# Kernel optimization log

Hardware: AMD Instinct MI355X
Metric: run time of the kernel (lower is better)

The kernel has to match this reference:

```python
import jax, jax.numpy as jnp
import numpy as np

NUM_HEADS = 16
ROPE_BASE = 10000.0

def rotate_half(x):
    h = x.shape[-1] // 2
    return jnp.concatenate([-x[..., h:], x[..., :h]], axis=-1)

def rope_cos_sin(seq_len, head_dim, dtype):
    inv_freq = 1.0 / (ROPE_BASE ** (jnp.arange(0, head_dim, 2, dtype=jnp.float32) / head_dim))
    t = jnp.arange(seq_len, dtype=jnp.float32)
    freqs = jnp.outer(t, inv_freq)              # [N, hd/2]
    emb = jnp.concatenate([freqs, freqs], -1)   # [N, hd]
    return jnp.cos(emb).astype(dtype), jnp.sin(emb).astype(dtype)

def setup_inputs() -> dict:
    key = jax.random.key(0)
    ks = jax.random.split(key, 5)
    B, N, D = 2, 2048, 1024
    s = 1.0 / np.sqrt(D)
    return {
        "x": jax.random.normal(ks[0], (B, N, D), jnp.float32),
        "attention_mask": jnp.ones((B, N), jnp.int32),
        "Wq": jax.random.normal(ks[1], (D, D), jnp.float32) * s,
        "Wk": jax.random.normal(ks[2], (D, D), jnp.float32) * s,
        "Wv": jax.random.normal(ks[3], (D, D), jnp.float32) * s,
        "Wo": jax.random.normal(ks[4], (D, D), jnp.float32) * s,
    }

def reference(x, attention_mask, Wq, Wk, Wv, Wo):
    B, N, D = x.shape
    H = NUM_HEADS
    hd = D // H
    scale = hd ** -0.5
    # projections (nn.Linear: x @ W.T), split heads -> [B, H, N, hd]
    q = jnp.einsum('bnd,ed->bne', x, Wq).reshape(B, N, H, hd).transpose(0, 2, 1, 3)
    k = jnp.einsum('bnd,ed->bne', x, Wk).reshape(B, N, H, hd).transpose(0, 2, 1, 3)
    v = jnp.einsum('bnd,ed->bne', x, Wv).reshape(B, N, H, hd).transpose(0, 2, 1, 3)
    cos, sin = rope_cos_sin(N, hd, x.dtype)     # [N, hd]
    cos = cos[None, None]; sin = sin[None, None]
    q = q * cos + rotate_half(q) * sin
    k = k * cos + rotate_half(k) * sin
    attn = jnp.einsum('bhqd,bhkd->bhqk', q, k) * scale
    mask = attention_mask.astype(bool)[:, None, None, :]        # [B,1,1,N]
    attn = jnp.where(mask, attn, -jnp.inf)
    all_masked = (attention_mask.sum(-1) == 0)[:, None, None, None]
    attn = jnp.where(all_masked, 0.0, attn)
    attn = jax.nn.softmax(attn, axis=-1)
    out = jnp.einsum('bhqk,bhkd->bhqd', attn, v)
    out = out.transpose(0, 2, 1, 3).reshape(B, N, D)
    return jnp.einsum('bnd,ed->bne', out, Wo)
```

## Files before the change

### kernel.cpp

```cpp
#include <hip/hip_runtime.h>
#include <math.h>

#define BATCH 2
#define SEQ   2048
#define DM    1024
#define NH    16
#define HD    64
#define MTOT  (BATCH*SEQ)

typedef short v8s __attribute__((ext_vector_type(8)));
typedef short v4s __attribute__((ext_vector_type(4)));
typedef float v4f __attribute__((ext_vector_type(4)));

#define MFMA16(a, b, c) __builtin_amdgcn_mfma_f32_16x16x32_bf16((a), (b), (c), 0, 0, 0)

__device__ __forceinline__ short f2b(float f) {
    union { float f; unsigned u; } v; v.f = f;
    return (short)((v.u + 0x8000u) >> 16);
}

__device__ __forceinline__ void rope_cs(int n, float f_rev, float* c, float* s) {
    float rev = (float)n * f_rev;
    float t = rev - floorf(rev);
    float ang = t * 6.283185307179586f;
    *c = __cosf(ang);
    *s = __sinf(ang);
}

#define L2_1E4_D32 0.4152410118609203f
#define INV2PI     0.15915494309189535f

__global__ __launch_bounds__(256) void cvt_all_kernel(
    const float* __restrict__ x,  const float* __restrict__ wq,
    const float* __restrict__ wk, const float* __restrict__ wv,
    const float* __restrict__ wo, short* __restrict__ dst)
{
    int i = blockIdx.x * 256 + threadIdx.x;
    const float* src; int off;
    if (i < (1 << 19)) { src = x; off = i; }
    else {
        int j = i - (1 << 19);
        int wsel = j >> 17;
        off = j & ((1 << 17) - 1);
        src = (wsel == 0) ? wq : (wsel == 1) ? wk : (wsel == 2) ? wv : wo;
    }
    const float4* s4 = (const float4*)src;
    float4 a = s4[2 * off], b = s4[2 * off + 1];
    v8s p;
    p[0] = f2b(a.x); p[1] = f2b(a.y); p[2] = f2b(a.z); p[3] = f2b(a.w);
    p[4] = f2b(b.x); p[5] = f2b(b.y); p[6] = f2b(b.z); p[7] = f2b(b.w);
    *(v8s*)&dst[8 * i] = p;
}

__global__ __launch_bounds__(256, 2) void kv_rope_mfma(
    const short* __restrict__ xb, const short* __restrict__ Wkb,
    const short* __restrict__ Wvb, short* __restrict__ K, short* __restrict__ Vt)
{
    const int zz = blockIdx.z;
    const short* __restrict__ Wb = zz ? Wvb : Wkb;
    const int m0 = blockIdx.x * 128, e00 = blockIdx.y * 128;
    const int tid = threadIdx.x;
    const int w = tid >> 6, lane = tid & 63, lq = lane >> 4, lr = lane & 15;
    const int wm = w >> 1, wn = w & 1;

    __shared__ union {
        struct { short As[128][32]; short Bs[128][32]; } p1;
        short Css[128][136];
    } u;

    v4f acc[4][4];
    #pragma unroll
    for (int i = 0; i < 4; ++i)
        for (int j = 0; j < 4; ++j)
            for (int r = 0; r < 4; ++r) acc[i][j][r] = 0.f;

    const int arow = tid >> 1, aseg = (tid & 1) * 16;
    for (int k0 = 0; k0 < DM; k0 += 32) {
        v8s a0 = *(const v8s*)&xb[(size_t)(m0 + arow) * DM + k0 + aseg];
        v8s a1 = *(const v8s*)&xb[(size_t)(m0 + arow) * DM + k0 + aseg + 8];
        v8s b0 = *(const v8s*)&Wb[(size_t)(e00 + arow) * DM + k0 + aseg];
        v8s b1 = *(const v8s*)&Wb[(size_t)(e00 + arow) * DM + k0 + aseg + 8];
        __syncthreads();
        *(v8s*)&u.p1.As[arow][aseg] = a0;
        *(v8s*)&u.p1.As[arow][aseg + 8] = a1;
        *(v8s*)&u.p1.Bs[arow][aseg] = b0;
        *(v8s*)&u.p1.Bs[arow][aseg + 8] = b1;
        __syncthreads();
        v8s af[4], bf[4];
        #pragma unroll
        for (int i = 0; i < 4; ++i)
            af[i] = *(const v8s*)&u.p1.As[64 * wm + 16 * i + lr][8 * lq];
        #pragma unroll
        for (int j = 0; j < 4; ++j)
            bf[j] = *(const v8s*)&u.p1.Bs[64 * wn + 16 * j + lr][8 * lq];
        #pragma unroll
        for (int i = 0; i < 4; ++i)
            #pragma unroll
            for (int j = 0; j < 4; ++j)
                acc[i][j] = MFMA16(af[i], bf[j], acc[i][j]);
    }
    __syncthreads();

    const int b = m0 >> 11, n00 = m0 & (SEQ - 1);

    if (zz == 0) {
        float f0 = exp2f(-(float)lr * L2_1E4_D32) * INV2PI;
        float f1 = exp2f(-(float)(16 + lr) * L2_1E4_D32) * INV2PI;
        #pragma unroll
        for (int i = 0; i < 4; ++i) {
            #pragma unroll
            for (int r = 0; r < 4; ++r) {
                int row = 64 * wm + 16 * i + 4 * lq + r;
                int n = n00 + row;
                float c0v, s0v, c1v, s1v;
                rope_cs(n, f0, &c0v, &s0v);
                rope_cs(n, f1, &c1v, &s1v);
                float q0 = acc[i][0][r], q1 = acc[i][1][r];
                float q2 = acc[i][2][r], q3 = acc[i][3][r];
                u.Css[row][64 * wn + lr]      = f2b(q0 * c0v - q2 * s0v);
                u.Css[row][64 * wn + 16 + lr] = f2b(q1 * c1v - q3 * s1v);
                u.Css[row][64 * wn + 32 + lr] = f2b(q2 * c0v + q0 * s0v);
                u.Css[row][64 * wn + 48 + lr] = f2b(q3 * c1v + q1 * s1v);
            }
        }
        __syncthreads();
        int row = tid >> 1, hh = tid & 1;
        int h = (e00 >> 6) + hh;
        int n = n00 + row;
        size_t base = (((size_t)(b * NH + h)) * SEQ + n) * HD;
        #pragma unroll
        for (int p = 0; p < 8; ++p)
            *(v8s*)&K[base + 8 * p] = *(const v8s*)&u.Css[row][64 * hh + 8 * p];
    } else {
        #pragma unroll
        for (int i = 0; i < 4; ++i) {
            #pragma unroll
            for (int j = 0; j < 4; ++j) {
                v4s t;
                #pragma unroll
                for (int r = 0; r < 4; ++r) t[r] = f2b(acc[i][j][r]);
                *(v4s*)&u.Css[64 * wn + 16 * j + lr][64 * wm + 16 * i + 4 * lq] = t;
            }
        }
        __syncthreads();
        int c = tid >> 1, half = (tid & 1) * 64;
        int h = (e00 + c) >> 6, d = (e00 + c) & 63;
        size_t base = (((size_t)(b * NH + h)) * HD + d) * SEQ + n00 + half;
        #pragma unroll
        for (int p = 0; p < 8; ++p)
            *(v8s*)&Vt[base + 8 * p] = *(const v8s*)&u.Css[c][half + 8 * p];
    }
}

__global__ __launch_bounds__(512, 4) void attn_mfma(
    const short* __restrict__ xb, const short* __restrict__ Wqb,
    const short* __restrict__ K, const short* __restrict__ Vt,
    const int* __restrict__ mask, short* __restrict__ O)
{
    const int m0 = blockIdx.x * 128, h = blockIdx.y, e0 = h * 64;
    const int b = m0 >> 11, n0 = m0 & (SEQ - 1), bh = b * NH + h;
    const int tid = threadIdx.x;
    const int w = tid >> 6, lane = tid & 63, lq = lane >> 4, lr = lane & 15;

    __shared__ union {
        struct { short As[128][32]; short Bs[64][32]; } p1;
        struct { short Ks[64][72]; short Vs[64][72]; } p2;
    } u;
    __shared__ short Ps[128][72];
    __shared__ float mbias[64];

    v4f acc[4];
    #pragma unroll
    for (int nt = 0; nt < 4; ++nt)
        for (int r = 0; r < 4; ++r) acc[nt][r] = 0.f;

    const int sr = tid >> 2, sc = (tid & 3) * 8;
    const int br = (tid - 256) >> 2, bc = (tid & 3) * 8;
    for (int k0 = 0; k0 < DM; k0 += 32) {
        v8s a0 = *(const v8s*)&xb[(size_t)(m0 + sr) * DM + k0 + sc];
        v8s bv;
        if (tid >= 256)
            bv = *(const v8s*)&Wqb[(size_t)(e0 + br) * DM + k0 + bc];
        __syncthreads();
        *(v8s*)&u.p1.As[sr][sc] = a0;
        if (tid >= 256)
            *(v8s*)&u.p1.Bs[br][bc] = bv;
        __syncthreads();
        v8s aw = *(const v8s*)&u.p1.As[16 * w + lr][8 * lq];
        #pragma unroll
        for (int nt = 0; nt < 4; ++nt) {
            v8s bb = *(const v8s*)&u.p1.Bs[16 * nt + lr][8 * lq];
            acc[nt] = MFMA16(aw, bb, acc[nt]);
        }
    }

    {
        const float QSCALE = 0.18033688011112042f;
        float f0 = exp2f(-(float)lr * L2_1E4_D32) * INV2PI;
        float f1 = exp2f(-(float)(16 + lr) * L2_1E4_D32) * INV2PI;
        #pragma unroll
        for (int r = 0; r < 4; ++r) {
            int row = 16 * w + 4 * lq + r;
            int n = n0 + row;
            float c0v, s0v, c1v, s1v;
            rope_cs(n, f0, &c0v, &s0v);
            rope_cs(n, f1, &c1v, &s1v);
            float q0 = acc[0][r], q1 = acc[1][r];
            float q2 = acc[2][r], q3 = acc[3][r];
            Ps[row][lr]      = f2b(QSCALE * (q0 * c0v - q2 * s0v));
            Ps[row][16 + lr] = f2b(QSCALE * (q1 * c1v - q3 * s1v));
            Ps[row][32 + lr] = f2b(QSCALE * (q2 * c0v + q0 * s0v));
            Ps[row][48 + lr] = f2b(QSCALE * (q3 * c1v + q1 * s1v));
        }
    }
    v8s aq[2];
    #pragma unroll
    for (int ks = 0; ks < 2; ++ks)
        aq[ks] = *(const v8s*)&Ps[16 * w + lr][32 * ks + 8 * lq];

    float lacc[4] = {0.f, 0.f, 0.f, 0.f};
    v4f o[4];
    #pragma unroll
    for (int nt = 0; nt < 4; ++nt)
        for (int r = 0; r < 4; ++r) o[nt][r] = 0.f;

    const int kr = tid >> 3, kc = (tid & 7) * 8;
    const int pr = 16 * (kr & 3) + (kr >> 2);
    const short* __restrict__ Kb = K + (size_t)bh * SEQ * HD;
    const short* __restrict__ Vb = Vt + (size_t)bh * HD * SEQ;

    v8s k1 = *(const v8s*)&Kb[(size_t)kr * HD + kc];
    v8s v1 = *(const v8s*)&Vb[(size_t)kr * SEQ + kc];
    int mnext = (tid < 64) ? mask[b * SEQ + tid] : 0;

    for (int c0 = 0; c0 < SEQ; c0 += 64) {
        __syncthreads();
        *(v8s*)&u.p2.Ks[pr][kc] = k1;
        *(v8s*)&u.p2.Vs[kr][kc] = v1;
        if (tid < 64) mbias[tid] = mnext ? -24.0f : -1e30f;
        __syncthreads();
        if (c0 + 64 < SEQ) {
            k1 = *(const v8s*)&Kb[(size_t)(c0 + 64 + kr) * HD + kc];
            v1 = *(const v8s*)&Vb[(size_t)kr * SEQ + c0 + 64 + kc];
            if (tid < 64) mnext = mask[b * SEQ + c0 + 64 + tid];
        }

        v8s kf[2][4], vf[2][4];
        #pragma unroll
        for (int ks = 0; ks < 2; ++ks)
            #pragma unroll
            for (int nt = 0; nt < 4; ++nt) {
                kf[ks][nt] = *(const v8s*)&u.p2.Ks[16 * nt + lr][32 * ks + 8 * lq];
                vf[ks][nt] = *(const v8s*)&u.p2.Vs[16 * nt + lr][32 * ks + 8 * lq];
            }
        float bias[4];
        #pragma unroll
        for (int nt = 0; nt < 4; ++nt) bias[nt] = mbias[4 * lr + nt];

        v4f sv[4];
        #pragma unroll
        for (int nt = 0; nt < 4; ++nt)
            for (int r = 0; r < 4; ++r) sv[nt][r] = 0.f;
        #pragma unroll
        for (int ks = 0; ks < 2; ++ks)
            #pragma unroll
            for (int nt = 0; nt < 4; ++nt)
                sv[nt] = MFMA16(aq[ks], kf[ks][nt], sv[nt]);

        #pragma unroll
        for (int r = 0; r < 4; ++r) {
            v4s pk;
            #pragma unroll
            for (int nt = 0; nt < 4; ++nt) {
                float p = exp2f(sv[nt][r] + bias[nt]);
                lacc[r] += p;
                pk[nt] = f2b(p);
            }
            *(v4s*)&Ps[16 * w + 4 * lq + r][4 * lr] = pk;
        }
        #pragma unroll
        for (int ks = 0; ks < 2; ++ks) {
            v8s a = *(const v8s*)&Ps[16 * w + lr][32 * ks + 8 * lq];
            #pragma unroll
            for (int nt = 0; nt < 4; ++nt)
                o[nt] = MFMA16(a, vf[ks][nt], o[nt]);
        }
    }

    #pragma unroll
    for (int r = 0; r < 4; ++r) {
        float l = lacc[r];
        l += __shfl_xor(l, 1);
        l += __shfl_xor(l, 2);
        l += __shfl_xor(l, 4);
        l += __shfl_xor(l, 8);
        float inv = (l > 0.f) ? 1.f / l : 0.f;
        int qrow = 16 * w + 4 * lq + r;
        #pragma unroll
        for (int nt = 0; nt < 4; ++nt)
            O[(size_t)(m0 + qrow) * DM + h * HD + 16 * nt + lr] =
                f2b(o[nt][r] * inv);
    }
}

__global__ __launch_bounds__(256, 2) void oproj_mfma(
    const short* __restrict__ O, const short* __restrict__ Wob,
    float* __restrict__ out)
{
    const int m0 = blockIdx.x * 64, e00 = blockIdx.y * 128;
    const int tid = threadIdx.x;
    const int w = tid >> 6, lane = tid & 63, lq = lane >> 4, lr = lane & 15;

    __shared__ short As[64][32];
    __shared__ short Bs[128][32];

    v4f acc[4][2];
    #pragma unroll
    for (int i = 0; i < 4; ++i)
        for (int j = 0; j < 2; ++j)
            for (int r = 0; r < 4; ++r) acc[i][j][r] = 0.f;

    const int arow = tid >> 2, aseg = (tid & 3) * 8;
    const int brow = tid >> 1, bseg = (tid & 1) * 16;
    for (int k0 = 0; k0 < DM; k0 += 32) {
        v8s a0 = *(const v8s*)&O[(size_t)(m0 + arow) * DM + k0 + aseg];
        v8s b0 = *(const v8s*)&Wob[(size_t)(e00 + brow) * DM + k0 + bseg];
        v8s b1 = *(const v8s*)&Wob[(size_t)(e00 + brow) * DM + k0 + bseg + 8];
        __syncthreads();
        *(v8s*)&As[arow][aseg] = a0;
        *(v8s*)&Bs[brow][bseg] = b0;
        *(v8s*)&Bs[brow][bseg + 8] = b1;
        __syncthreads();
        v8s af[4], bf[2];
        #pragma unroll
        for (int i = 0; i < 4; ++i)
            af[i] = *(const v8s*)&As[16 * i + lr][8 * lq];
        #pragma unroll
        for (int j = 0; j < 2; ++j)
            bf[j] = *(const v8s*)&Bs[32 * w + 16 * j + lr][8 * lq];
        #pragma unroll
        for (int i = 0; i < 4; ++i)
            #pragma unroll
            for (int j = 0; j < 2; ++j)
                acc[i][j] = MFMA16(af[i], bf[j], acc[i][j]);
    }

    #pragma unroll
    for (int i = 0; i < 4; ++i)
        #pragma unroll
        for (int r = 0; r < 4; ++r) {
            int m = m0 + 16 * i + 4 * lq + r;
            #pragma unroll
            for (int j = 0; j < 2; ++j)
                out[(size_t)m * DM + e00 + 32 * w + 16 * j + lr] = acc[i][j][r];
        }
}

extern "C" void kernel_launch(void* const* d_in, const int* in_sizes, int n_in,
                              void* d_out, int out_size, void* d_ws, size_t ws_size,
                              hipStream_t stream)
{
    const float* x    = (const float*)d_in[0];
    const int*   mask = (const int*)d_in[1];
    const float* Wq   = (const float*)d_in[2];
    const float* Wk   = (const float*)d_in[3];
    const float* Wv   = (const float*)d_in[4];
    const float* Wo   = (const float*)d_in[5];
    float* out = (float*)d_out;

    short* xb  = (short*)d_ws;
    short* Wqb = xb  + (size_t)MTOT * DM;
    short* Wkb = Wqb + (size_t)DM * DM;
    short* Wvb = Wkb + (size_t)DM * DM;
    short* Wob = Wvb + (size_t)DM * DM;
    short* O   = Wob + (size_t)DM * DM;
    short* K  = (short*)d_out;
    short* Vt = K + (size_t)MTOT * DM;

    cvt_all_kernel<<<4096, 256, 0, stream>>>(x, Wq, Wk, Wv, Wo, xb);

    dim3 g1(MTOT / 128, DM / 128, 2);
    kv_rope_mfma<<<g1, 256, 0, stream>>>(xb, Wkb, Wvb, K, Vt);

    dim3 g2(MTOT / 128, NH);
    attn_mfma<<<g2, 512, 0, stream>>>(xb, Wqb, K, Vt, mask, O);

    dim3 g3(MTOT / 64, DM / 128);
    oproj_mfma<<<g3, 256, 0, stream>>>(O, Wob, out);
}
```

Before: 218.9 us.

## Move Q projection into batched QKV GEMM and widen attention KV tiles to 128

The Q projection and its RoPE/scale step move out of the attention kernel into the shared projection kernel as a third grid slice, so attention now reads a precomputed, pre-scaled Q from workspace. The attention loop now stages 128 keys per iteration instead of 64, processed in two halves, which halves the number of barrier pairs and global load rounds. O reuses the xb buffer to save workspace. The cost is an extra round-trip of Q through global memory, larger LDS use in attention, and a launch-bounds occupancy hint of 3 on the projection kernel.

```diff
diff --git a/kernel.cpp b/kernel.cpp
--- a/kernel.cpp
+++ b/kernel.cpp
@@ -29,6 +29,7 @@
 
 #define L2_1E4_D32 0.4152410118609203f
 #define INV2PI     0.15915494309189535f
+#define QSCALE     0.18033688011112042f
 
 __global__ __launch_bounds__(256) void cvt_all_kernel(
     const float* __restrict__ x,  const float* __restrict__ wq,
@@ -52,12 +53,13 @@
     *(v8s*)&dst[8 * i] = p;
 }
 
-__global__ __launch_bounds__(256, 2) void kv_rope_mfma(
-    const short* __restrict__ xb, const short* __restrict__ Wkb,
-    const short* __restrict__ Wvb, short* __restrict__ K, short* __restrict__ Vt)
+__global__ __launch_bounds__(256, 3) void qkv_rope_mfma(
+    const short* __restrict__ xb, const short* __restrict__ Wqb,
+    const short* __restrict__ Wkb, const short* __restrict__ Wvb,
+    short* __restrict__ K, short* __restrict__ Vt, short* __restrict__ Qb)
 {
     const int zz = blockIdx.z;
-    const short* __restrict__ Wb = zz ? Wvb : Wkb;
+    const short* __restrict__ Wb = (zz == 0) ? Wkb : (zz == 1) ? Wvb : Wqb;
     const int m0 = blockIdx.x * 128, e00 = blockIdx.y * 128;
     const int tid = threadIdx.x;
     const int w = tid >> 6, lane = tid & 63, lq = lane >> 4, lr = lane & 15;
@@ -103,7 +105,9 @@
 
     const int b = m0 >> 11, n00 = m0 & (SEQ - 1);
 
-    if (zz == 0) {
+    if (zz != 1) {
+        short* __restrict__ dst = (zz == 0) ? K : Qb;
+        const float sc = (zz == 0) ? 1.0f : QSCALE;
         float f0 = exp2f(-(float)lr * L2_1E4_D32) * INV2PI;
         float f1 = exp2f(-(float)(16 + lr) * L2_1E4_D32) * INV2PI;
         #pragma unroll
@@ -117,10 +121,10 @@
                 rope_cs(n, f1, &c1v, &s1v);
                 float q0 = acc[i][0][r], q1 = acc[i][1][r];
                 float q2 = acc[i][2][r], q3 = acc[i][3][r];
-                u.Css[row][64 * wn + lr]      = f2b(q0 * c0v - q2 * s0v);
-                u.Css[row][64 * wn + 16 + lr] = f2b(q1 * c1v - q3 * s1v);
-                u.Css[row][64 * wn + 32 + lr] = f2b(q2 * c0v + q0 * s0v);
-                u.Css[row][64 * wn + 48 + lr] = f2b(q3 * c1v + q1 * s1v);
+                u.Css[row][64 * wn + lr]      = f2b(sc * (q0 * c0v - q2 * s0v));
+                u.Css[row][64 * wn + 16 + lr] = f2b(sc * (q1 * c1v - q3 * s1v));
+                u.Css[row][64 * wn + 32 + lr] = f2b(sc * (q2 * c0v + q0 * s0v));
+                u.Css[row][64 * wn + 48 + lr] = f2b(sc * (q3 * c1v + q1 * s1v));
             }
         }
         __syncthreads();
@@ -130,7 +134,7 @@
         size_t base = (((size_t)(b * NH + h)) * SEQ + n) * HD;
         #pragma unroll
         for (int p = 0; p < 8; ++p)
-            *(v8s*)&K[base + 8 * p] = *(const v8s*)&u.Css[row][64 * hh + 8 * p];
+            *(v8s*)&dst[base + 8 * p] = *(const v8s*)&u.Css[row][64 * hh + 8 * p];
     } else {
         #pragma unroll
         for (int i = 0; i < 4; ++i) {
@@ -153,70 +157,25 @@
 }
 
 __global__ __launch_bounds__(512, 4) void attn_mfma(
-    const short* __restrict__ xb, const short* __restrict__ Wqb,
-    const short* __restrict__ K, const short* __restrict__ Vt,
-    const int* __restrict__ mask, short* __restrict__ O)
-{
-    const int m0 = blockIdx.x * 128, h = blockIdx.y, e0 = h * 64;
+    const short* __restrict__ Qb, const short* __restrict__ K,
+    const short* __restrict__ Vt, const int* __restrict__ mask,
+    short* __restrict__ O)
+{
+    const int m0 = blockIdx.x * 128, h = blockIdx.y;
     const int b = m0 >> 11, n0 = m0 & (SEQ - 1), bh = b * NH + h;
     const int tid = threadIdx.x;
     const int w = tid >> 6, lane = tid & 63, lq = lane >> 4, lr = lane & 15;
 
-    __shared__ union {
-        struct { short As[128][32]; short Bs[64][32]; } p1;
-        struct { short Ks[64][72]; short Vs[64][72]; } p2;
-    } u;
+    __shared__ short Ks[128][72];
+    __shared__ short Vs[64][136];
     __shared__ short Ps[128][72];
-    __shared__ float mbias[64];
-
-    v4f acc[4];
-    #pragma unroll
-    for (int nt = 0; nt < 4; ++nt)
-        for (int r = 0; r < 4; ++r) acc[nt][r] = 0.f;
-
-    const int sr = tid >> 2, sc = (tid & 3) * 8;
-    const int br = (tid - 256) >> 2, bc = (tid & 3) * 8;
-    for (int k0 = 0; k0 < DM; k0 += 32) {
-        v8s a0 = *(const v8s*)&xb[(size_t)(m0 + sr) * DM + k0 + sc];
-        v8s bv;
-        if (tid >= 256)
-            bv = *(const v8s*)&Wqb[(size_t)(e0 + br) * DM + k0 + bc];
-        __syncthreads();
-        *(v8s*)&u.p1.As[sr][sc] = a0;
-        if (tid >= 256)
-            *(v8s*)&u.p1.Bs[br][bc] = bv;
-        __syncthreads();
-        v8s aw = *(const v8s*)&u.p1.As[16 * w + lr][8 * lq];
-        #pragma unroll
-        for (int nt = 0; nt < 4; ++nt) {
-            v8s bb = *(const v8s*)&u.p1.Bs[16 * nt + lr][8 * lq];
-            acc[nt] = MFMA16(aw, bb, acc[nt]);
-        }
-    }
-
-    {
-        const float QSCALE = 0.18033688011112042f;
-        float f0 = exp2f(-(float)lr * L2_1E4_D32) * INV2PI;
-        float f1 = exp2f(-(float)(16 + lr) * L2_1E4_D32) * INV2PI;
-        #pragma unroll
-        for (int r = 0; r < 4; ++r) {
-            int row = 16 * w + 4 * lq + r;
-            int n = n0 + row;
-            float c0v, s0v, c1v, s1v;
-            rope_cs(n, f0, &c0v, &s0v);
-            rope_cs(n, f1, &c1v, &s1v);
-            float q0 = acc[0][r], q1 = acc[1][r];
-            float q2 = acc[2][r], q3 = acc[3][r];
-            Ps[row][lr]      = f2b(QSCALE * (q0 * c0v - q2 * s0v));
-            Ps[row][16 + lr] = f2b(QSCALE * (q1 * c1v - q3 * s1v));
-            Ps[row][32 + lr] = f2b(QSCALE * (q2 * c0v + q0 * s0v));
-            Ps[row][48 + lr] = f2b(QSCALE * (q3 * c1v + q1 * s1v));
-        }
-    }
+    __shared__ float mbias[128];
+
+    const short* __restrict__ Qh = Qb + (size_t)bh * SEQ * HD;
     v8s aq[2];
     #pragma unroll
     for (int ks = 0; ks < 2; ++ks)
-        aq[ks] = *(const v8s*)&Ps[16 * w + lr][32 * ks + 8 * lq];
+        aq[ks] = *(const v8s*)&Qh[(size_t)(n0 + 16 * w + lr) * HD + 32 * ks + 8 * lq];
 
     float lacc[4] = {0.f, 0.f, 0.f, 0.f};
     v4f o[4];
@@ -224,66 +183,77 @@
     for (int nt = 0; nt < 4; ++nt)
         for (int r = 0; r < 4; ++r) o[nt][r] = 0.f;
 
-    const int kr = tid >> 3, kc = (tid & 7) * 8;
-    const int pr = 16 * (kr & 3) + (kr >> 2);
+    const int kr = tid >> 2, kc = (tid & 3) * 16;
+    const int krh = kr & 63;
+    const int pkr = 64 * (kr >> 6) + 16 * (krh & 3) + (krh >> 2);
+    const int vr = tid >> 3, vc = (tid & 7) * 16;
     const short* __restrict__ Kb = K + (size_t)bh * SEQ * HD;
     const short* __restrict__ Vb = Vt + (size_t)bh * HD * SEQ;
 
     v8s k1 = *(const v8s*)&Kb[(size_t)kr * HD + kc];
-    v8s v1 = *(const v8s*)&Vb[(size_t)kr * SEQ + kc];
-    int mnext = (tid < 64) ? mask[b * SEQ + tid] : 0;
-
-    for (int c0 = 0; c0 < SEQ; c0 += 64) {
-        __syncthreads();
-        *(v8s*)&u.p2.Ks[pr][kc] = k1;
-        *(v8s*)&u.p2.Vs[kr][kc] = v1;
-        if (tid < 64) mbias[tid] = mnext ? -24.0f : -1e30f;
-        __syncthreads();
-        if (c0 + 64 < SEQ) {
-            k1 = *(const v8s*)&Kb[(size_t)(c0 + 64 + kr) * HD + kc];
-            v1 = *(const v8s*)&Vb[(size_t)kr * SEQ + c0 + 64 + kc];
-            if (tid < 64) mnext = mask[b * SEQ + c0 + 64 + tid];
-        }
-
-        v8s kf[2][4], vf[2][4];
-        #pragma unroll
-        for (int ks = 0; ks < 2; ++ks)
-            #pragma unroll
-            for (int nt = 0; nt < 4; ++nt) {
-                kf[ks][nt] = *(const v8s*)&u.p2.Ks[16 * nt + lr][32 * ks + 8 * lq];
-                vf[ks][nt] = *(const v8s*)&u.p2.Vs[16 * nt + lr][32 * ks + 8 * lq];
+    v8s k2 = *(const v8s*)&Kb[(size_t)kr * HD + kc + 8];
+    v8s v1 = *(const v8s*)&Vb[(size_t)vr * SEQ + vc];
+    v8s v2 = *(const v8s*)&Vb[(size_t)vr * SEQ + vc + 8];
+    int mnext = (tid < 128) ? mask[b * SEQ + tid] : 0;
+
+    for (int c0 = 0; c0 < SEQ; c0 += 128) {
+        __syncthreads();
+        *(v8s*)&Ks[pkr][kc] = k1;
+        *(v8s*)&Ks[pkr][kc + 8] = k2;
+        *(v8s*)&Vs[vr][vc] = v1;
+        *(v8s*)&Vs[vr][vc + 8] = v2;
+        if (tid < 128) mbias[tid] = mnext ? -24.0f : -1e30f;
+        __syncthreads();
+        if (c0 + 128 < SEQ) {
+            k1 = *(const v8s*)&Kb[(size_t)(c0 + 128 + kr) * HD + kc];
+            k2 = *(const v8s*)&Kb[(size_t)(c0 + 128 + kr) * HD + kc + 8];
+            v1 = *(const v8s*)&Vb[(size_t)vr * SEQ + c0 + 128 + vc];
+            v2 = *(const v8s*)&Vb[(size_t)vr * SEQ + c0 + 128 + vc + 8];
+            if (tid < 128) mnext = mask[b * SEQ + c0 + 128 + tid];
+        }
+
+        #pragma unroll
+        for (int half = 0; half < 2; ++half) {
+            v8s kf[2][4];
+            #pragma unroll
+            for (int ks = 0; ks < 2; ++ks)
+                #pragma unroll
+                for (int nt = 0; nt < 4; ++nt)
+                    kf[ks][nt] = *(const v8s*)&Ks[64 * half + 16 * nt + lr][32 * ks + 8 * lq];
+            float bias[4];
+            #pragma unroll
+            for (int nt = 0; nt < 4; ++nt) bias[nt] = mbias[64 * half + 4 * lr + nt];
+
+            v4f sv[4];
+            #pragma unroll
+            for (int nt = 0; nt < 4; ++nt)
+                for (int r = 0; r < 4; ++r) sv[nt][r] = 0.f;
+            #pragma unroll
+            for (int ks = 0; ks < 2; ++ks)
+                #pragma unroll
+                for (int nt = 0; nt < 4; ++nt)
+                    sv[nt] = MFMA16(aq[ks], kf[ks][nt], sv[nt]);
+
+            #pragma unroll
+            for (int r = 0; r < 4; ++r) {
+                v4s pk;
+                #pragma unroll
+                for (int nt = 0; nt < 4; ++nt) {
+                    float p = exp2f(sv[nt][r] + bias[nt]);
+                    lacc[r] += p;
+                    pk[nt] = f2b(p);
+                }
+                *(v4s*)&Ps[16 * w + 4 * lq + r][4 * lr] = pk;
             }
-        float bias[4];
-        #pragma unroll
-        for (int nt = 0; nt < 4; ++nt) bias[nt] = mbias[4 * lr + nt];
-
-        v4f sv[4];
-        #pragma unroll
-        for (int nt = 0; nt < 4; ++nt)
-            for (int r = 0; r < 4; ++r) sv[nt][r] = 0.f;
-        #pragma unroll
-        for (int ks = 0; ks < 2; ++ks)
-            #pragma unroll
-            for (int nt = 0; nt < 4; ++nt)
-                sv[nt] = MFMA16(aq[ks], kf[ks][nt], sv[nt]);
-
-        #pragma unroll
-        for (int r = 0; r < 4; ++r) {
-            v4s pk;
-            #pragma unroll
-            for (int nt = 0; nt < 4; ++nt) {
-                float p = exp2f(sv[nt][r] + bias[nt]);
-                lacc[r] += p;
-                pk[nt] = f2b(p);
+            #pragma unroll
+            for (int ks = 0; ks < 2; ++ks) {
+                v8s a = *(const v8s*)&Ps[16 * w + lr][32 * ks + 8 * lq];
+                #pragma unroll
+                for (int nt = 0; nt < 4; ++nt) {
+                    v8s vf = *(const v8s*)&Vs[16 * nt + lr][64 * half + 32 * ks + 8 * lq];
+                    o[nt] = MFMA16(a, vf, o[nt]);
+                }
             }
-            *(v4s*)&Ps[16 * w + 4 * lq + r][4 * lr] = pk;
-        }
-        #pragma unroll
-        for (int ks = 0; ks < 2; ++ks) {
-            v8s a = *(const v8s*)&Ps[16 * w + lr][32 * ks + 8 * lq];
-            #pragma unroll
-            for (int nt = 0; nt < 4; ++nt)
-                o[nt] = MFMA16(a, vf[ks][nt], o[nt]);
         }
     }
 
@@ -373,17 +343,18 @@
     short* Wkb = Wqb + (size_t)DM * DM;
     short* Wvb = Wkb + (size_t)DM * DM;
     short* Wob = Wvb + (size_t)DM * DM;
-    short* O   = Wob + (size_t)DM * DM;
+    short* Qb  = Wob + (size_t)DM * DM;
+    short* O   = xb;
     short* K  = (short*)d_out;
     short* Vt = K + (size_t)MTOT * DM;
 
     cvt_all_kernel<<<4096, 256, 0, stream>>>(x, Wq, Wk, Wv, Wo, xb);
 
-    dim3 g1(MTOT / 128, DM / 128, 2);
-    kv_rope_mfma<<<g1, 256, 0, stream>>>(xb, Wkb, Wvb, K, Vt);
+    dim3 g1(MTOT / 128, DM / 128, 3);
+    qkv_rope_mfma<<<g1, 256, 0, stream>>>(xb, Wqb, Wkb, Wvb, K, Vt, Qb);
 
     dim3 g2(MTOT / 128, NH);
-    attn_mfma<<<g2, 512, 0, stream>>>(xb, Wqb, K, Vt, mask, O);
+    attn_mfma<<<g2, 512, 0, stream>>>(Qb, K, Vt, mask, O);
 
     dim3 g3(MTOT / 64, DM / 128);
     oproj_mfma<<<g3, 256, 0, stream>>>(O, Wob, out);
```

New measurement: 211.6 us. 1.03x faster.
